# Performance work log

Measured on AMD Instinct MI355X. Metric: run time of the kernel, lower is better.

## Reference

```python
import jax, jax.numpy as jnp
import numpy as np

B, C_IN, H, W = 8, 256, 32, 32
DK = 256
DV = 256
NH = 8
DKH = DK // NH  # 32
C_OUT = 512
KS, PAD = 3, 1


def setup_inputs() -> dict:
    key = jax.random.key(0)
    ks = jax.random.split(key, 9)
    s = 0.05
    return {
        "x": jax.random.normal(ks[0], (B, C_IN, H, W), jnp.float32),
        "w_qkv": jax.random.normal(ks[1], (2 * DK + DV, C_IN, 1, 1), jnp.float32) * s,
        "b_qkv": jnp.zeros((2 * DK + DV,), jnp.float32),
        "w_attn": jax.random.normal(ks[2], (DV, DV, 1, 1), jnp.float32) * s,
        "b_attn": jnp.zeros((DV,), jnp.float32),
        "w_out": jax.random.normal(ks[3], (C_OUT - DV, C_IN, KS, KS), jnp.float32) * s,
        "b_out": jnp.zeros((C_OUT - DV,), jnp.float32),
        # torch init: dkh**-0.5 + rand
        "key_rel_w": DKH ** (-0.5) + jax.random.uniform(ks[4], (2 * W - 1, DKH), jnp.float32),
        "key_rel_h": DKH ** (-0.5) + jax.random.uniform(ks[5], (2 * H - 1, DKH), jnp.float32),
    }


def conv2d(x, w, b, pad):
    y = jax.lax.conv_general_dilated(
        x, w, window_strides=(1, 1), padding=[(pad, pad), (pad, pad)],
        dimension_numbers=("NCHW", "OIHW", "NCHW"))
    return y + b[None, :, None, None]


def rel_to_abs(x):
    # x: [b, nh, L, 2L-1] -> [b, nh, L, L] (skew trick)
    b, nh, L, _ = x.shape
    x = jnp.pad(x, ((0, 0), (0, 0), (0, 0), (0, 1)))
    flat = x.reshape(b, nh, L * 2 * L)
    flat = jnp.pad(flat, ((0, 0), (0, 0), (0, L - 1)))
    final = flat.reshape(b, nh, L + 1, 2 * L - 1)
    return final[:, :, :L, L - 1:]


def relative_logits_1d(q, rel_k, Hd, Wd, transpose_mask):
    # q: [B, NH, DKH, Hd, Wd]; rel_k: [2*Wd-1, DKH]
    rel = jnp.einsum("bhdxy,md->bhxym", q, rel_k)          # [B,NH,Hd,Wd,2Wd-1]
    rel = rel.reshape(-1, NH * Hd, Wd, 2 * Wd - 1)
    rel = rel_to_abs(rel)                                   # [B,NH*Hd,Wd,Wd]
    rel = rel.reshape(-1, NH, Hd, 1, Wd, Wd)
    rel = jnp.broadcast_to(rel, (rel.shape[0], NH, Hd, Hd, Wd, Wd))
    rel = jnp.transpose(rel, transpose_mask)
    return rel.reshape(-1, NH, Hd * Wd, Hd * Wd)


def reference(x, w_qkv, b_qkv, w_attn, b_attn, w_out, b_out, key_rel_w, key_rel_h):
    conv_out = conv2d(x, w_out, b_out, PAD)                 # [B, C_OUT-DV, H, W]
    qkv = conv2d(x, w_qkv, b_qkv, 0)                        # [B, 2DK+DV, H, W]
    q, k, v = jnp.split(qkv, [DK, 2 * DK], axis=1)
    q = q.reshape(B, NH, DKH, H * W) * (DKH ** -0.5)        # scaled BEFORE rel logits (as in torch)
    k = k.reshape(B, NH, DKH, H * W)
    v = v.reshape(B, NH, DV // NH, H * W)
    logits = jnp.einsum("bhdl,bhdm->bhlm", q, k)            # [B,NH,HW,HW]
    q5 = q.reshape(B, NH, DKH, H, W)
    w_rel = relative_logits_1d(q5, key_rel_w, H, W, (0, 1, 2, 4, 3, 5))
    h_rel = relative_logits_1d(jnp.transpose(q5, (0, 1, 2, 4, 3)), key_rel_h, W, H, (0, 1, 4, 2, 5, 3))
    logits = logits + h_rel + w_rel
    weights = jax.nn.softmax(logits, axis=-1)
    attn = jnp.einsum("bhlm,bhdm->bhdl", weights, v)        # [B,NH,DVH,HW]
    attn = attn.reshape(B, DV, H, W)
    attn = conv2d(attn, w_attn, b_attn, 0)
    return jnp.concatenate([conv_out, attn], axis=1)        # [B, C_OUT, H, W]
```

## Files before the change

kernel.cpp:

```cpp
#include <hip/hip_runtime.h>
#include <hip/hip_bf16.h>


typedef __hip_bfloat16 bf16;
typedef __attribute__((ext_vector_type(8))) short bf16x8;
typedef __attribute__((ext_vector_type(4))) float f32x4;

__device__ __forceinline__ float blo(unsigned int v) { return __uint_as_float(v << 16); }
__device__ __forceinline__ float bhi(unsigned int v) { return __uint_as_float(v & 0xffff0000u); }
__device__ __forceinline__ unsigned short f2bfbits(float f) {
  union { bf16 h; unsigned short u; } cv; cv.h = __float2bfloat16(f); return cv.u;
}
__device__ __forceinline__ unsigned int cvt_pk_bf16(float lo, float hi) {
  unsigned int r;
  asm("v_cvt_pk_bf16_f32 %0, %1, %2" : "=v"(r) : "v"(lo), "v"(hi));
  return r;
}
__device__ __forceinline__ float exp2_f(float x) {
#if __has_builtin(__builtin_amdgcn_exp2f)
  return __builtin_amdgcn_exp2f(x);
#else
  return exp2f(x);
#endif
}

__global__ __launch_bounds__(256) void prep_kernel(
    const float* __restrict__ x, const float* __restrict__ wout,
    bf16* __restrict__ xT, bf16* __restrict__ wob0, bf16* __restrict__ wob1)
{
  int bid = blockIdx.x, tid = threadIdx.x;
  if (bid < 2048) {
    __shared__ float t[32 * 33];
    int b = bid >> 8, rem = bid & 255;
    int ci0 = (rem >> 5) * 32, l0 = (rem & 31) * 32;
    {
      int ciL = tid >> 3, lL4 = (tid & 7) * 4;
      float4 v = *(const float4*)(x + (size_t)(b * 256 + ci0 + ciL) * 1024 + l0 + lL4);
      t[ciL * 33 + lL4 + 0] = v.x; t[ciL * 33 + lL4 + 1] = v.y;
      t[ciL * 33 + lL4 + 2] = v.z; t[ciL * 33 + lL4 + 3] = v.w;
    }
    __syncthreads();
    {
      int lL = tid >> 3, cS = (tid & 7) * 4;
      unsigned int p0 = (unsigned int)f2bfbits(t[(cS + 0) * 33 + lL]) |
                        ((unsigned int)f2bfbits(t[(cS + 1) * 33 + lL]) << 16);
      unsigned int p1 = (unsigned int)f2bfbits(t[(cS + 2) * 33 + lL]) |
                        ((unsigned int)f2bfbits(t[(cS + 3) * 33 + lL]) << 16);
      uint2 u2; u2.x = p0; u2.y = p1;
      *(uint2*)(xT + ((size_t)(b * 1024) + l0 + lL) * 256 + ci0 + cS) = u2;
    }
  } else {
    int t0 = (bid - 2048) * 256 + tid;
#pragma unroll
    for (int s = 0; s < 8; ++s) {
      int u = s * 9216 + t0;
      int chunkblk = u / 2304;
      int within = u - chunkblk * 2304;
      int co63 = within / 36;
      int r = within - co63 * 36;
      int kidx = r >> 2, cig = r & 3;
      int co = (chunkblk >> 3) * 64 + co63;
      int ci = (chunkblk & 7) * 32 + cig * 8;
      union { unsigned short h[8]; uint4 u4; } pk;
#pragma unroll
      for (int j = 0; j < 8; ++j)
        pk.h[j] = f2bfbits(wout[(size_t)(co * 256 + ci + j) * 9 + kidx]);
      bf16* dst = (chunkblk < 28) ? (wob0 + (size_t)chunkblk * 18432)
                                  : (wob1 + (size_t)(chunkblk - 28) * 18432);
      *(uint4*)(dst + (size_t)within * 8) = pk.u4;
    }
  }
}

__global__ __launch_bounds__(256) void convqkv_kernel(
    const bf16* __restrict__ xT,
    const bf16* __restrict__ wob0, const bf16* __restrict__ wob1,
    const float* __restrict__ b_out, float* __restrict__ out,
    const float* __restrict__ wq, const float* __restrict__ b_qkv,
    bf16* __restrict__ qT, bf16* __restrict__ kR, bf16* __restrict__ vW)
{
  __shared__ __align__(16) short smem[27104];
  int tid = threadIdx.x, lane = tid & 63, wave = tid >> 6;
  int m16 = lane & 15, quad = lane >> 4;

  if (blockIdx.x < 256) {
    short* wS = smem;
    short* xS = smem + 18944;
    int bid = blockIdx.x;
    int rc = bid & 7, cotile = (bid >> 3) & 3, b = bid >> 5;
    int y0 = rc * 4;

    f32x4 acc[8];
#pragma unroll
    for (int t = 0; t < 8; ++t) acc[t] = (f32x4){0.f, 0.f, 0.f, 0.f};

    for (int ck = 0; ck < 8; ++ck) {
      __syncthreads();
      int cb = cotile * 8 + ck;
      const bf16* wbase = (cb < 28) ? (wob0 + (size_t)cb * 18432)
                                    : (wob1 + (size_t)(cb - 28) * 18432);
#pragma unroll
      for (int r = 0; r < 9; ++r) {
        int u = r * 256 + tid;
        *(uint4*)(wS + (u / 36) * 296 + (u % 36) * 8) = *(const uint4*)(wbase + (size_t)u * 8);
      }
#pragma unroll
      for (int r = 0; r < 3; ++r) {
        int u = r * 256 + tid;
        int pos = u >> 2, seg = u & 3;
        int row = pos >> 5, col = pos & 31;
        int gy = y0 - 1 + row;
        uint4 val = make_uint4(0u, 0u, 0u, 0u);
        if (gy >= 0 && gy < 32)
          val = *(const uint4*)(xT + ((size_t)(b * 1024) + gy * 32 + col) * 256 + ck * 32 + seg * 8);
        *(uint4*)(xS + (row * 34 + col + 1) * 40 + seg * 8) = val;
      }
      if (tid < 48) {
        int pos = tid >> 2, seg = tid & 3;
        int row = pos >> 1, side = pos & 1;
        *(uint4*)(xS + (row * 34 + side * 33) * 40 + seg * 8) = make_uint4(0u, 0u, 0u, 0u);
      }
      __syncthreads();
#pragma unroll
      for (int kidx = 0; kidx < 9; ++kidx) {
        int dy = kidx / 3, dx = kidx - dy * 3;
        bf16x8 af = *(const bf16x8*)(wS + (wave * 16 + m16) * 296 + kidx * 32 + quad * 8);
#pragma unroll
        for (int t = 0; t < 8; ++t) {
          int row = (t >> 1) + dy;
          int col = (t & 1) * 16 + m16 + dx;
          bf16x8 bf = *(const bf16x8*)(xS + (row * 34 + col) * 40 + quad * 8);
          acc[t] = __builtin_amdgcn_mfma_f32_16x16x32_bf16(af, bf, acc[t], 0, 0, 0);
        }
      }
    }

    int cob = cotile * 64 + wave * 16 + quad * 4;
#pragma unroll
    for (int i = 0; i < 4; ++i) {
      float bv = b_out[cob + i];
#pragma unroll
      for (int t = 0; t < 8; ++t) {
        int y = y0 + (t >> 1), xc = (t & 1) * 16 + m16;
        out[((size_t)(b * 512) + cob + i) * 1024 + y * 32 + xc] = acc[t][i] + bv;
      }
    }
  } else {
    short* aS = smem;
    short* bS = smem + 4608;
    int bid2 = blockIdx.x - 256;
    int ltile = bid2 & 7;
    int rest = bid2 >> 3;
    int ctile = rest % 12;
    int b = rest / 12;
    int l0 = ltile * 128;
    int cbase = ctile * 64;

    f32x4 acc[8];
#pragma unroll
    for (int t = 0; t < 8; ++t) acc[t] = (f32x4){0.f, 0.f, 0.f, 0.f};

    for (int ck = 0; ck < 4; ++ck) {
      __syncthreads();
#pragma unroll
      for (int r = 0; r < 4; ++r) {
        int u = r * 256 + tid;
        int c = u >> 4, s4 = u & 15;
        float4 v = *(const float4*)(wq + (size_t)(cbase + c) * 256 + ck * 64 + s4 * 4);
        unsigned int p0 = (unsigned int)f2bfbits(v.x) | ((unsigned int)f2bfbits(v.y) << 16);
        unsigned int p1 = (unsigned int)f2bfbits(v.z) | ((unsigned int)f2bfbits(v.w) << 16);
        uint2 u2; u2.x = p0; u2.y = p1;
        *(uint2*)(aS + c * 72 + s4 * 4) = u2;
      }
#pragma unroll
      for (int r = 0; r < 4; ++r) {
        int u = r * 256 + tid;
        int l = u >> 3, seg = u & 7;
        *(uint4*)(bS + l * 72 + seg * 8) =
            *(const uint4*)(xT + ((size_t)(b * 1024) + l0 + l) * 256 + ck * 64 + seg * 8);
      }
      __syncthreads();
#pragma unroll
      for (int ks = 0; ks < 2; ++ks) {
        bf16x8 af = *(const bf16x8*)(aS + (wave * 16 + m16) * 72 + ks * 32 + quad * 8);
#pragma unroll
        for (int t = 0; t < 8; ++t) {
          bf16x8 bf = *(const bf16x8*)(bS + (t * 16 + m16) * 72 + ks * 32 + quad * 8);
          acc[t] = __builtin_amdgcn_mfma_f32_16x16x32_bf16(af, bf, acc[t], 0, 0, 0);
        }
      }
    }

    __syncthreads();
    short* ldsT = smem + wave * 3072;
    int cb = cbase + wave * 16;
    bool isq = (ctile < 4);
    float bv[4];
#pragma unroll
    for (int i = 0; i < 4; ++i) bv[i] = b_qkv[cb + quad * 4 + i];
#pragma unroll
    for (int t = 0; t < 8; ++t) {
#pragma unroll
      for (int i = 0; i < 4; ++i) {
        float v = acc[t][i] + bv[i];
        if (isq) v *= 0.17677669529663689f;
        ldsT[(t * 16 + m16) * 24 + quad * 4 + i] = (short)f2bfbits(v);
      }
    }
    if (ctile < 8) {
      bf16* dst = isq ? qT : kR;
      int coff = isq ? cb : cb - 256;
#pragma unroll
      for (int rep = 0; rep < 4; ++rep) {
        int u = rep * 64 + lane;
        int l = u >> 1, half = u & 1;
        int c0 = coff + half * 8;
        int head = b * 8 + (c0 >> 5), d0 = c0 & 31;
        *(uint4*)(dst + ((size_t)head * 1024 + l0 + l) * 32 + d0) =
            *(const uint4*)(ldsT + l * 24 + half * 8);
      }
    } else {
      int dcol = lane >> 2, lg = lane & 3;
      int c2 = (cb - 512) + dcol;
      int head = b * 8 + (c2 >> 5), gd = c2 & 31;
      int dt = gd >> 4, m16v = gd & 15;
      int cch = ltile * 2 + (lg >> 1);
      int ksv = lg & 1;
      bf16* vbase = vW + (size_t)head * 32768 + cch * 2048 + (dt * 2 + ksv) * 512 + m16v * 8;
#pragma unroll
      for (int s = 0; s < 4; ++s) {
#pragma unroll
        for (int p = 0; p < 4; ++p) {
          int j0 = lg * 32 + s * 8 + p * 2;
          unsigned int u0 = (unsigned short)ldsT[j0 * 24 + dcol];
          unsigned int u1 = (unsigned short)ldsT[(j0 + 1) * 24 + dcol];
          unsigned int w = u0 | (u1 << 16);
          int quadp = (s & 1) * 2 + (p >> 1);
          int jj = (p & 1) * 2 + (s >> 1) * 4;
          *(unsigned int*)(vbase + quadp * 128 + jj) = w;
        }
      }
    }
  }
}

__global__ __launch_bounds__(256) void attn_mfma_kernel(
    const bf16* __restrict__ qT, const bf16* __restrict__ kR, const bf16* __restrict__ vW,
    const float* __restrict__ krw, const float* __restrict__ krh,
    bf16* __restrict__ attL)
{
  __shared__ __align__(16) char smem[27648];
  float* stgF = (float*)smem;
  float* rhS  = (float*)(smem + 9728);
  float* rwS  = (float*)(smem + 18432);

  const float L2E = 1.4426950408889634f;

  int tid = threadIdx.x;
  int lane = tid & 63, wave = tid >> 6;
  int m16 = lane & 15, quad = lane >> 4;
  int bid = blockIdx.x;
  int head = ((bid & 7) << 3) | ((bid >> 3) & 7);
  int qt = bid >> 6;
  int row0 = qt * 64;
  int b = head >> 3, h = head & 7;

  int r = tid >> 2, jseg = tid & 3;
  float q32[32];
  {
    const bf16* qp = qT + ((size_t)head * 1024 + row0 + r) * 32;
#pragma unroll
    for (int s4 = 0; s4 < 4; ++s4) {
      uint4 u = ((const uint4*)qp)[s4];
      q32[s4 * 8 + 0] = blo(u.x); q32[s4 * 8 + 1] = bhi(u.x);
      q32[s4 * 8 + 2] = blo(u.y); q32[s4 * 8 + 3] = bhi(u.y);
      q32[s4 * 8 + 4] = blo(u.z); q32[s4 * 8 + 5] = bhi(u.z);
      q32[s4 * 8 + 6] = blo(u.w); q32[s4 * 8 + 7] = bhi(u.w);
    }
  }

  for (int i = tid; i < 504; i += 256) {
    int row = i >> 3, d0 = (i & 7) * 4;
    *(float4*)(stgF + row * 36 + d0) = *(const float4*)(krw + row * 32 + d0);
  }
  __syncthreads();

  {
    int qi = r & 31;
#pragma unroll
    for (int jj2 = 0; jj2 < 2; ++jj2) {
      float rv[4];
#pragma unroll
      for (int jp = 0; jp < 4; ++jp) {
        int j = jseg * 8 + jj2 * 4 + jp;
        const float* kw = stgF + (j - qi + 31) * 36;
        float s1 = 0.f;
#pragma unroll
        for (int d4 = 0; d4 < 8; ++d4) {
          float4 kv = *(const float4*)(kw + d4 * 4);
          s1 += q32[d4 * 4 + 0] * kv.x + q32[d4 * 4 + 1] * kv.y +
                q32[d4 * 4 + 2] * kv.z + q32[d4 * 4 + 3] * kv.w;
        }
        rv[jp] = s1 * L2E;
      }
      *(float4*)(rwS + r * 36 + jseg * 8 + jj2 * 4) = make_float4(rv[0], rv[1], rv[2], rv[3]);
    }
  }
  __syncthreads();

  for (int i = tid; i < 504; i += 256) {
    int row = i >> 3, d0 = (i & 7) * 4;
    *(float4*)(stgF + row * 36 + d0) = *(const float4*)(krh + row * 32 + d0);
  }
  __syncthreads();

  {
    int qy = qt * 2 + (r >> 5);
#pragma unroll
    for (int jj = 0; jj < 8; ++jj) {
      int j = jseg * 8 + jj;
      const float* kh = stgF + (j - qy + 31) * 36;
      float s2 = 0.f;
#pragma unroll
      for (int d4 = 0; d4 < 8; ++d4) {
        float4 kv = *(const float4*)(kh + d4 * 4);
        s2 += q32[d4 * 4 + 0] * kv.x + q32[d4 * 4 + 1] * kv.y +
              q32[d4 * 4 + 2] * kv.z + q32[d4 * 4 + 3] * kv.w;
      }
      rhS[j * 68 + r] = s2 * L2E;
    }
  }
  __syncthreads();

  bf16x8 afrag = *(const bf16x8*)(
      qT + ((size_t)head * 1024 + row0 + wave * 16 + m16) * 32 + quad * 8);
  float rwreg[2][4];
  {
    float4 rw0 = *(const float4*)(rwS + (wave * 16 + m16) * 36 + quad * 4);
    float4 rw1 = *(const float4*)(rwS + (wave * 16 + m16) * 36 + 16 + quad * 4);
    rwreg[0][0] = rw0.x; rwreg[0][1] = rw0.y; rwreg[0][2] = rw0.z; rwreg[0][3] = rw0.w;
    rwreg[1][0] = rw1.x; rwreg[1][1] = rw1.y; rwreg[1][2] = rw1.z; rwreg[1][3] = rw1.w;
  }

  const bf16* kp = kR + (size_t)head * 32768 + m16 * 32 + quad * 8;
  const bf16* vp = vW + (size_t)head * 32768 + lane * 8;

  f32x4 oacc[2];
  oacc[0] = (f32x4){0.f, 0.f, 0.f, 0.f};
  oacc[1] = (f32x4){0.f, 0.f, 0.f, 0.f};
  float rsp = 0.f;

#pragma unroll 1
  for (int c = 0; c < 16; ++c) {
    union { uint4 u; bf16x8 v; } kf[4], vf[4];
#pragma unroll
    for (int t = 0; t < 4; ++t)
      kf[t].u = *(const uint4*)(kp + c * 2048 + t * 512);
#pragma unroll
    for (int q = 0; q < 4; ++q)
      vf[q].u = *(const uint4*)(vp + c * 2048 + q * 512);

    float rh0 = rhS[(c * 2 + 0) * 68 + wave * 16 + m16];
    float rh1 = rhS[(c * 2 + 1) * 68 + wave * 16 + m16];

    f32x4 sacc[4];
#pragma unroll
    for (int t = 0; t < 4; ++t) {
      f32x4 z = (f32x4){0.f, 0.f, 0.f, 0.f};
      sacc[t] = __builtin_amdgcn_mfma_f32_16x16x32_bf16(kf[t].v, afrag, z, 0, 0, 0);
    }

    unsigned int pk[4][2];
#pragma unroll
    for (int t = 0; t < 4; ++t) {
      float rh = (t < 2) ? rh0 : rh1;
      float e0 = exp2_f(fmaf(sacc[t][0], L2E, rwreg[t & 1][0] + rh));
      float e1 = exp2_f(fmaf(sacc[t][1], L2E, rwreg[t & 1][1] + rh));
      float e2 = exp2_f(fmaf(sacc[t][2], L2E, rwreg[t & 1][2] + rh));
      float e3 = exp2_f(fmaf(sacc[t][3], L2E, rwreg[t & 1][3] + rh));
      rsp += (e0 + e1) + (e2 + e3);
      pk[t][0] = cvt_pk_bf16(e0, e1);
      pk[t][1] = cvt_pk_bf16(e2, e3);
    }

#pragma unroll
    for (int ks = 0; ks < 2; ++ks) {
      union { unsigned int w[4]; bf16x8 v; } pf;
      pf.w[0] = pk[2 * ks][0];     pf.w[1] = pk[2 * ks][1];
      pf.w[2] = pk[2 * ks + 1][0]; pf.w[3] = pk[2 * ks + 1][1];
#pragma unroll
      for (int dt = 0; dt < 2; ++dt) {
        oacc[dt] = __builtin_amdgcn_mfma_f32_16x16x32_bf16(vf[dt * 2 + ks].v, pf.v, oacc[dt], 0, 0, 0);
      }
    }
  }

  rsp += __shfl_xor(rsp, 16, 64);
  rsp += __shfl_xor(rsp, 32, 64);
  float invs = 1.0f / rsp;
  int grow = row0 + wave * 16 + m16;
#pragma unroll
  for (int dt = 0; dt < 2; ++dt) {
    uint2 st;
    st.x = cvt_pk_bf16(oacc[dt][0] * invs, oacc[dt][1] * invs);
    st.y = cvt_pk_bf16(oacc[dt][2] * invs, oacc[dt][3] * invs);
    *(uint2*)(attL + ((size_t)b * 1024 + grow) * 256 + h * 32 + dt * 16 + quad * 4) = st;
  }
}

__global__ __launch_bounds__(256) void attnout_mfma_kernel(
    const bf16* __restrict__ attL, const float* __restrict__ w, const float* __restrict__ bias,
    float* __restrict__ out)
{
  __shared__ __align__(16) short smem[13824];
  short* aS = smem;
  short* bS = smem + 4608;

  int tid = threadIdx.x, lane = tid & 63, wave = tid >> 6;
  int m16 = lane & 15, quad = lane >> 4;
  int l0 = blockIdx.x * 128;
  int cotile = blockIdx.y;
  int b = blockIdx.z;
  int cbase = cotile * 64;

  f32x4 acc[8];
#pragma unroll
  for (int t = 0; t < 8; ++t) acc[t] = (f32x4){0.f, 0.f, 0.f, 0.f};

  for (int ck = 0; ck < 4; ++ck) {
    __syncthreads();
#pragma unroll
    for (int r = 0; r < 4; ++r) {
      int u = r * 256 + tid;
      int c = u >> 4, s4 = u & 15;
      float4 v = *(const float4*)(w + (size_t)(cbase + c) * 256 + ck * 64 + s4 * 4);
      unsigned int p0 = (unsigned int)f2bfbits(v.x) | ((unsigned int)f2bfbits(v.y) << 16);
      unsigned int p1 = (unsigned int)f2bfbits(v.z) | ((unsigned int)f2bfbits(v.w) << 16);
      uint2 u2; u2.x = p0; u2.y = p1;
      *(uint2*)(aS + c * 72 + s4 * 4) = u2;
    }
#pragma unroll
    for (int r = 0; r < 4; ++r) {
      int u = r * 256 + tid;
      int l = u >> 3, seg = u & 7;
      *(uint4*)(bS + l * 72 + seg * 8) =
          *(const uint4*)(attL + ((size_t)(b * 1024) + l0 + l) * 256 + ck * 64 + seg * 8);
    }
    __syncthreads();
#pragma unroll
    for (int ks = 0; ks < 2; ++ks) {
      bf16x8 af = *(const bf16x8*)(aS + (wave * 16 + m16) * 72 + ks * 32 + quad * 8);
#pragma unroll
      for (int t = 0; t < 8; ++t) {
        bf16x8 bf = *(const bf16x8*)(bS + (t * 16 + m16) * 72 + ks * 32 + quad * 8);
        acc[t] = __builtin_amdgcn_mfma_f32_16x16x32_bf16(af, bf, acc[t], 0, 0, 0);
      }
    }
  }

  int co = cbase + wave * 16 + quad * 4;
#pragma unroll
  for (int i = 0; i < 4; ++i) {
    float bv = bias[co + i];
    size_t obase = ((size_t)(b * 512) + 256 + co + i) * 1024 + l0;
#pragma unroll
    for (int t = 0; t < 8; ++t)
      out[obase + t * 16 + m16] = acc[t][i] + bv;
  }
}

extern "C" void kernel_launch(void* const* d_in, const int* in_sizes, int n_in,
                              void* d_out, int out_size, void* d_ws, size_t ws_size,
                              hipStream_t stream) {
  const float* x      = (const float*)d_in[0];
  const float* w_qkv  = (const float*)d_in[1];
  const float* b_qkv  = (const float*)d_in[2];
  const float* w_attn = (const float*)d_in[3];
  const float* b_attn = (const float*)d_in[4];
  const float* w_out  = (const float*)d_in[5];
  const float* b_out  = (const float*)d_in[6];
  const float* krw    = (const float*)d_in[7];
  const float* krh    = (const float*)d_in[8];
  float* out = (float*)d_out;

  bf16* ws    = (bf16*)d_ws;
  bf16* xT    = ws;
  bf16* attL  = ws;
  bf16* qT    = ws + 2097152;
  bf16* kR    = ws + 4194304;
  bf16* vF    = ws + 6291456;

  bf16* wob0 = (bf16*)(out + (size_t)(0 * 512 + 256) * 1024);
  bf16* wob1 = (bf16*)(out + (size_t)(1 * 512 + 256) * 1024);

  prep_kernel<<<dim3(2084), 256, 0, stream>>>(x, w_out, xT, wob0, wob1);
  convqkv_kernel<<<dim3(1024), 256, 0, stream>>>(xT, wob0, wob1, b_out, out,
                                                 w_qkv, b_qkv, qT, kR, vF);
  attn_mfma_kernel<<<dim3(1024), 256, 0, stream>>>(qT, kR, vF, krw, krh, attL);
  attnout_mfma_kernel<<<dim3(8, 4, 8), 256, 0, stream>>>(attL, w_attn, b_attn, out);
}
```

Measured before the change: 147.8 us.

## Compute relative position logits with MFMA instead of scalar FP32 dot products

Replaces the per-thread FP32 dot products of q against key_rel_w and key_rel_h with bf16 MFMA tiles. Each block computes the full 63x64 table of relative logits per axis into LDS, then gathers the skewed entries each query needs. This removes two LDS staging passes, several barriers and the scalar FMA work in the prologue. In exchange the relative embeddings are rounded to bf16, which lowers the precision of the bias terms, and LDS use per block grows.

After: 145.0 us. Within noise of the previous version (-1.9%).

```diff
diff --git a/kernel.cpp b/kernel.cpp
--- a/kernel.cpp
+++ b/kernel.cpp
@@ -249,10 +249,9 @@
     const float* __restrict__ krw, const float* __restrict__ krh,
     bf16* __restrict__ attL)
 {
-  __shared__ __align__(16) char smem[27648];
-  float* stgF = (float*)smem;
-  float* rhS  = (float*)(smem + 9728);
-  float* rwS  = (float*)(smem + 18432);
+  __shared__ __align__(16) char smem[34816];
+  float* RWf = (float*)smem;
+  float* RHf = (float*)(smem + 17408);
 
   const float L2E = 1.4426950408889634f;
 
@@ -265,82 +264,54 @@
   int row0 = qt * 64;
   int b = head >> 3, h = head & 7;
 
-  int r = tid >> 2, jseg = tid & 3;
-  float q32[32];
   {
-    const bf16* qp = qT + ((size_t)head * 1024 + row0 + r) * 32;
-#pragma unroll
-    for (int s4 = 0; s4 < 4; ++s4) {
-      uint4 u = ((const uint4*)qp)[s4];
-      q32[s4 * 8 + 0] = blo(u.x); q32[s4 * 8 + 1] = bhi(u.x);
-      q32[s4 * 8 + 2] = blo(u.y); q32[s4 * 8 + 3] = bhi(u.y);
-      q32[s4 * 8 + 4] = blo(u.z); q32[s4 * 8 + 5] = bhi(u.z);
-      q32[s4 * 8 + 6] = blo(u.w); q32[s4 * 8 + 7] = bhi(u.w);
-    }
-  }
-
-  for (int i = tid; i < 504; i += 256) {
-    int row = i >> 3, d0 = (i & 7) * 4;
-    *(float4*)(stgF + row * 36 + d0) = *(const float4*)(krw + row * 32 + d0);
-  }
-  __syncthreads();
-
-  {
-    int qi = r & 31;
-#pragma unroll
-    for (int jj2 = 0; jj2 < 2; ++jj2) {
-      float rv[4];
-#pragma unroll
-      for (int jp = 0; jp < 4; ++jp) {
-        int j = jseg * 8 + jj2 * 4 + jp;
-        const float* kw = stgF + (j - qi + 31) * 36;
-        float s1 = 0.f;
-#pragma unroll
-        for (int d4 = 0; d4 < 8; ++d4) {
-          float4 kv = *(const float4*)(kw + d4 * 4);
-          s1 += q32[d4 * 4 + 0] * kv.x + q32[d4 * 4 + 1] * kv.y +
-                q32[d4 * 4 + 2] * kv.z + q32[d4 * 4 + 3] * kv.w;
-        }
-        rv[jp] = s1 * L2E;
-      }
-      *(float4*)(rwS + r * 36 + jseg * 8 + jj2 * 4) = make_float4(rv[0], rv[1], rv[2], rv[3]);
-    }
-  }
-  __syncthreads();
-
-  for (int i = tid; i < 504; i += 256) {
-    int row = i >> 3, d0 = (i & 7) * 4;
-    *(float4*)(stgF + row * 36 + d0) = *(const float4*)(krh + row * 32 + d0);
-  }
-  __syncthreads();
-
-  {
-    int qy = qt * 2 + (r >> 5);
-#pragma unroll
-    for (int jj = 0; jj < 8; ++jj) {
-      int j = jseg * 8 + jj;
-      const float* kh = stgF + (j - qy + 31) * 36;
-      float s2 = 0.f;
-#pragma unroll
-      for (int d4 = 0; d4 < 8; ++d4) {
-        float4 kv = *(const float4*)(kh + d4 * 4);
-        s2 += q32[d4 * 4 + 0] * kv.x + q32[d4 * 4 + 1] * kv.y +
-              q32[d4 * 4 + 2] * kv.z + q32[d4 * 4 + 3] * kv.w;
-      }
-      rhS[j * 68 + r] = s2 * L2E;
+    int mrow = wave * 16 + m16;
+    bool valid = (mrow < 63);
+    float4 w0 = make_float4(0.f, 0.f, 0.f, 0.f), w1 = w0, h0 = w0, h1 = w0;
+    if (valid) {
+      w0 = *(const float4*)(krw + mrow * 32 + quad * 8);
+      w1 = *(const float4*)(krw + mrow * 32 + quad * 8 + 4);
+      h0 = *(const float4*)(krh + mrow * 32 + quad * 8);
+      h1 = *(const float4*)(krh + mrow * 32 + quad * 8 + 4);
+    }
+    union { unsigned int w[4]; bf16x8 v; } aw, ah;
+    aw.w[0] = cvt_pk_bf16(w0.x * L2E, w0.y * L2E);
+    aw.w[1] = cvt_pk_bf16(w0.z * L2E, w0.w * L2E);
+    aw.w[2] = cvt_pk_bf16(w1.x * L2E, w1.y * L2E);
+    aw.w[3] = cvt_pk_bf16(w1.z * L2E, w1.w * L2E);
+    ah.w[0] = cvt_pk_bf16(h0.x * L2E, h0.y * L2E);
+    ah.w[1] = cvt_pk_bf16(h0.z * L2E, h0.w * L2E);
+    ah.w[2] = cvt_pk_bf16(h1.x * L2E, h1.y * L2E);
+    ah.w[3] = cvt_pk_bf16(h1.z * L2E, h1.w * L2E);
+#pragma unroll
+    for (int nt = 0; nt < 4; ++nt) {
+      bf16x8 qf = *(const bf16x8*)(
+          qT + ((size_t)head * 1024 + row0 + nt * 16 + m16) * 32 + quad * 8);
+      f32x4 z = (f32x4){0.f, 0.f, 0.f, 0.f};
+      f32x4 dw = __builtin_amdgcn_mfma_f32_16x16x32_bf16(aw.v, qf, z, 0, 0, 0);
+      f32x4 dh = __builtin_amdgcn_mfma_f32_16x16x32_bf16(ah.v, qf, z, 0, 0, 0);
+#pragma unroll
+      for (int i = 0; i < 4; ++i) {
+        int mr = wave * 16 + quad * 4 + i;
+        RWf[mr * 68 + nt * 16 + m16] = dw[i];
+        RHf[mr * 68 + nt * 16 + m16] = dh[i];
+      }
     }
   }
   __syncthreads();
 
   bf16x8 afrag = *(const bf16x8*)(
       qT + ((size_t)head * 1024 + row0 + wave * 16 + m16) * 32 + quad * 8);
+  int qloc = wave * 16 + m16;
+  int qm = qloc & 31;
   float rwreg[2][4];
-  {
-    float4 rw0 = *(const float4*)(rwS + (wave * 16 + m16) * 36 + quad * 4);
-    float4 rw1 = *(const float4*)(rwS + (wave * 16 + m16) * 36 + 16 + quad * 4);
-    rwreg[0][0] = rw0.x; rwreg[0][1] = rw0.y; rwreg[0][2] = rw0.z; rwreg[0][3] = rw0.w;
-    rwreg[1][0] = rw1.x; rwreg[1][1] = rw1.y; rwreg[1][2] = rw1.z; rwreg[1][3] = rw1.w;
-  }
+#pragma unroll
+  for (int par = 0; par < 2; ++par)
+#pragma unroll
+    for (int i = 0; i < 4; ++i)
+      rwreg[par][i] = RWf[(par * 16 + quad * 4 + i - qm + 31) * 68 + qloc];
+  int qy = qt * 2 + (qloc >> 5);
+  const float* rhp = RHf + (31 - qy) * 68 + qloc;
 
   const bf16* kp = kR + (size_t)head * 32768 + m16 * 32 + quad * 8;
   const bf16* vp = vW + (size_t)head * 32768 + lane * 8;
@@ -360,8 +331,8 @@
     for (int q = 0; q < 4; ++q)
       vf[q].u = *(const uint4*)(vp + c * 2048 + q * 512);
 
-    float rh0 = rhS[(c * 2 + 0) * 68 + wave * 16 + m16];
-    float rh1 = rhS[(c * 2 + 1) * 68 + wave * 16 + m16];
+    float rh0 = rhp[(c * 2 + 0) * 68];
+    float rh1 = rhp[(c * 2 + 1) * 68];
 
     f32x4 sacc[4];
 #pragma unroll
```
